# Kernel optimization log

Measured on AMD Instinct MI355X. Metric: run time of the kernel, lower is better.

Reference implementation:

```python
import jax, jax.numpy as jnp
import numpy as np

# Channel schedule of FPSRefineNet(num_structure_points=64, in_channel=640, out=False):
# 640->512 (ReLU), 512->256 (ReLU), 256->128 (ReLU), 128->64 (ReLU since out=False)
CH = [640, 512, 256, 128, 64]
BN_EPS = 1e-5


def _conv_bn_relu(x, W, b, g, beta, m, v):
    # 1x1 Conv2d over [B,C,K,S] == channel matmul; BN in eval mode (running stats);
    # dropout is identity in eval.
    x = jnp.einsum('oc,bcks->boks', W, x) + b[None, :, None, None]
    inv = g / jnp.sqrt(v + BN_EPS)
    x = x * inv[None, :, None, None] + (beta - m * inv)[None, :, None, None]
    return jax.nn.relu(x)


def setup_inputs() -> dict:
    key = jax.random.key(0)
    ks = jax.random.split(key, 32)
    d = {}
    d['grouped_xyz'] = jax.random.normal(ks[0], (8, 3, 32, 1024), jnp.float32)
    d['grouped_points'] = jax.random.normal(ks[1], (8, 640, 32, 1024), jnp.float32)
    i = 2
    for li, (cin, cout) in enumerate(zip(CH[:-1], CH[1:])):
        d[f'W{li}'] = jax.random.normal(ks[i], (cout, cin), jnp.float32) / np.sqrt(cin).astype(np.float32); i += 1
        d[f'b{li}'] = jnp.zeros((cout,), jnp.float32)
        d[f'g{li}'] = jnp.ones((cout,), jnp.float32)
        d[f'beta{li}'] = jnp.zeros((cout,), jnp.float32)
        d[f'm{li}'] = 0.1 * jax.random.normal(ks[i], (cout,), jnp.float32); i += 1
        d[f'v{li}'] = 1.0 + 0.1 * jax.random.uniform(ks[i], (cout,), jnp.float32); i += 1
    return d


def reference(grouped_xyz, grouped_points,
              W0, b0, g0, beta0, m0, v0,
              W1, b1, g1, beta1, m1, v1,
              W2, b2, g2, beta2, m2, v2,
              W3, b3, g3, beta3, m3, v3):
    params = [(W0, b0, g0, beta0, m0, v0),
              (W1, b1, g1, beta1, m1, v1),
              (W2, b2, g2, beta2, m2, v2),
              (W3, b3, g3, beta3, m3, v3)]
    x = grouped_points  # [B, 640, K, S]
    for (W, b, g, be, m, v) in params:
        x = _conv_bn_relu(x, W, b, g, be, m, v)
    # softmax over K (dim=2)
    p = jax.nn.softmax(x, axis=2)  # [B, D'=64, K, S]
    # fused weighted sum over K: sum_k p[b,d,k,s]*xyz[b,c,k,s] -> [B, C, D', S]
    offset_xyz = jnp.einsum('bdks,bcks->bcds', p, grouped_xyz)
    return offset_xyz
```

## Files before the change

### kernel.cpp

```cpp
#include <hip/hip_runtime.h>

typedef unsigned short u16;
typedef __attribute__((ext_vector_type(8))) short bf16x8;
typedef __attribute__((ext_vector_type(4))) float f32x4;
typedef __attribute__((ext_vector_type(16))) float f32x16;

__device__ __forceinline__ u16 f2bf(float f) {
  union { float f; unsigned u; } x; x.f = f;
  return (u16)((x.u + 0x7FFFu + ((x.u >> 16) & 1u)) >> 16);
}
__device__ __forceinline__ float bf2f(u16 h) {
  union { unsigned u; float f; } x; x.u = ((unsigned)h) << 16; return x.f;
}
__device__ __forceinline__ unsigned cvtpk(float lo, float hi) {
  unsigned r;
  asm("v_cvt_pk_bf16_f32 %0, %1, %2" : "=v"(r) : "v"(lo), "v"(hi));
  return r;
}


__global__ __launch_bounds__(256) void prep_kernel(
    const float* __restrict__ W0, const float* __restrict__ W1,
    const float* __restrict__ W2, const float* __restrict__ W3,
    const float* __restrict__ b0, const float* __restrict__ g0, const float* __restrict__ be0, const float* __restrict__ m0, const float* __restrict__ v0,
    const float* __restrict__ b1, const float* __restrict__ g1, const float* __restrict__ be1, const float* __restrict__ m1, const float* __restrict__ v1,
    const float* __restrict__ b2, const float* __restrict__ g2, const float* __restrict__ be2, const float* __restrict__ m2, const float* __restrict__ v2,
    const float* __restrict__ b3, const float* __restrict__ g3, const float* __restrict__ be3, const float* __restrict__ m3, const float* __restrict__ v3,
    u16* __restrict__ Wb, float* __restrict__ sc, float* __restrict__ sh)
{
  int i = blockIdx.x * 256 + threadIdx.x;
  if (i < 62464) {
    const float* Ws; int CIN, KS, local, dstb; bool f16 = false;
    if (i < 40960)      { local = i;         Ws = W0; CIN = 640; KS = 40; dstb = 0; }
    else if (i < 57344) { local = i - 40960; Ws = W1; CIN = 512; KS = 32; dstb = 327680; }
    else if (i < 61440) { local = i - 57344; Ws = W2; CIN = 256; KS = 16; dstb = 458752; }
    else                { local = i - 61440; Ws = W3; CIN = 128; KS = 4;  dstb = 491520; f16 = true; }
    int lane = local & 63, fi = local >> 6;
    int ks = fi % KS, mt = fi / KS;
    int row, k;
    if (!f16) { row = mt * 32 + (lane & 31); k = ks * 16 + (lane >> 5) * 8; }
    else      { row = mt * 16 + (lane & 15); k = ks * 32 + (lane >> 4) * 8; }
    const float* s = Ws + (size_t)row * CIN + k;
    bf16x8 pk;
    #pragma unroll
    for (int j = 0; j < 8; ++j) pk[j] = (short)f2bf(s[j]);
    *reinterpret_cast<bf16x8*>(Wb + dstb + (size_t)local * 8) = pk;
  }
  if (i < 960) {
    const float *B, *G, *BE, *M, *V; int c;
    if (i < 512)      { c = i;       B = b0; G = g0; BE = be0; M = m0; V = v0; }
    else if (i < 768) { c = i - 512; B = b1; G = g1; BE = be1; M = m1; V = v1; }
    else if (i < 896) { c = i - 768; B = b2; G = g2; BE = be2; M = m2; V = v2; }
    else              { c = i - 896; B = b3; G = g3; BE = be3; M = m3; V = v3; }
    float inv = G[c] / sqrtf(V[c] + 1e-5f);
    sc[i] = inv;
    sh[i] = (B[c] - M[c]) * inv + BE[c];
  }
}

template<int MT, int NT>
__device__ __forceinline__ void store_act32(f32x16 (&acc)[MT][NT],
    const float* __restrict__ sc, const float* __restrict__ sh,
    int mrow0, int ntb, int lane, u16* __restrict__ dst, int rowB)
{
  const int l31 = lane & 31, khalf = lane >> 5;
  #pragma unroll
  for (int mi = 0; mi < MT; ++mi) {
    #pragma unroll
    for (int rq = 0; rq < 4; ++rq) {
      const int ch0 = mrow0 + mi * 32 + rq * 8 + khalf * 4;
      const f32x4 s4 = *reinterpret_cast<const f32x4*>(sc + ch0);
      const f32x4 h4 = *reinterpret_cast<const f32x4*>(sh + ch0);
      #pragma unroll
      for (int nt = 0; nt < NT; ++nt) {
        const int px = (ntb + nt) * 32 + l31;
        float r0 = fmaxf(acc[mi][nt][rq * 4 + 0] * s4[0] + h4[0], 0.f);
        float r1 = fmaxf(acc[mi][nt][rq * 4 + 1] * s4[1] + h4[1], 0.f);
        float r2 = fmaxf(acc[mi][nt][rq * 4 + 2] * s4[2] + h4[2], 0.f);
        float r3 = fmaxf(acc[mi][nt][rq * 4 + 3] * s4[3] + h4[3], 0.f);
        uint2 pk;
        pk.x = cvtpk(r0, r1);
        pk.y = cvtpk(r2, r3);
        const unsigned byte = ((unsigned)(px * rowB + ch0 * 2)) ^ ((unsigned)((px & 7) << 4));
        *reinterpret_cast<uint2*>(reinterpret_cast<char*>(dst) + byte) = pk;
      }
    }
  }
}

__device__ __forceinline__ void load8(const float* __restrict__ gbase, int choff, float (&v)[8]) {
  const float* s = gbase + (size_t)choff * 32768u;
  #pragma unroll
  for (int kk = 0; kk < 8; ++kk) v[kk] = s[(size_t)kk * 32768u];
}
__device__ __forceinline__ void write8(float (&v)[8], char* __restrict__ buf, unsigned wb) {
  uint4 pk;
  pk.x = cvtpk(v[0], v[1]);
  pk.y = cvtpk(v[2], v[3]);
  pk.z = cvtpk(v[4], v[5]);
  pk.w = cvtpk(v[6], v[7]);
  *reinterpret_cast<uint4*>(buf + wb) = pk;
}

#define P0_HALF(XB, c, ks0) { \
  __builtin_amdgcn_s_setprio(1); \
  _Pragma("unroll") \
  for (int ksl = 0; ksl < 4; ++ksl) { \
    const int ks = (ks0) + ksl; \
    const unsigned base = ((unsigned)(l31 * 256 + ks * 32 + khalf * 16)) ^ sw; \
    bf16x8 bb0 = *reinterpret_cast<const bf16x8*>((XB) + base); \
    bf16x8 bb1 = *reinterpret_cast<const bf16x8*>((XB) + base + 8192); \
    const int slot = ks & 1; \
    acc0[0][0] = __builtin_amdgcn_mfma_f32_32x32x16_bf16(ar0[slot], bb0, acc0[0][0], 0, 0, 0); \
    acc0[0][1] = __builtin_amdgcn_mfma_f32_32x32x16_bf16(ar0[slot], bb1, acc0[0][1], 0, 0, 0); \
    acc0[1][0] = __builtin_amdgcn_mfma_f32_32x32x16_bf16(ar1[slot], bb0, acc0[1][0], 0, 0, 0); \
    acc0[1][1] = __builtin_amdgcn_mfma_f32_32x32x16_bf16(ar1[slot], bb1, acc0[1][1], 0, 0, 0); \
    const int g_ = (c) * 8 + ks + 2; \
    if (g_ < 40) { \
      ar0[slot] = *reinterpret_cast<const bf16x8*>(A0 + g_ * 512); \
      ar1[slot] = *reinterpret_cast<const bf16x8*>(A1 + g_ * 512); \
    } \
  } \
  __builtin_amdgcn_s_setprio(0); \
}

__global__ __launch_bounds__(512, 4) void fused4_kernel(
    const float* __restrict__ gp, const u16* __restrict__ Wb,
    const float* __restrict__ sc, const float* __restrict__ sh,
    u16* __restrict__ x3)
{
  __shared__ u16 smem[32768];
  char* XsA = reinterpret_cast<char*>(smem);
  char* XsB = XsA + 16384;
  u16*  Y0s = smem;

  const int tid  = threadIdx.x;
  const int lane = tid & 63;
  const int w    = tid >> 6;
  const int l31  = lane & 31, khalf = lane >> 5;
  const unsigned sw = (unsigned)((l31 & 7) << 4);

  const int b  = blockIdx.x >> 9;
  const int jt = blockIdx.x & 511;
  const int j0 = jt << 6;

  const float* gbase = gp + (size_t)b * (640u * 32768u) + (unsigned)(j0 + lane);
  const unsigned wbH0 = ((unsigned)(lane * 256 + w * 16)) ^ ((unsigned)((lane & 7) << 4));
  const unsigned wbH1 = wbH0 + 128;

  const u16* A0 = Wb + (size_t)(2 * w) * (40 * 512) + lane * 8;
  const u16* A1 = A0 + (size_t)(40 * 512);

  float vA[8], vB[8];
  bf16x8 ar0[2], ar1[2];
  f32x16 acc0[2][2] = {};

  load8(gbase, 0 * 128 + 0 * 64 + w * 8, vA);
  load8(gbase, 0 * 128 + 1 * 64 + w * 8, vB);
  ar0[0] = *reinterpret_cast<const bf16x8*>(A0 + 0 * 512);
  ar1[0] = *reinterpret_cast<const bf16x8*>(A1 + 0 * 512);
  ar0[1] = *reinterpret_cast<const bf16x8*>(A0 + 1 * 512);
  ar1[1] = *reinterpret_cast<const bf16x8*>(A1 + 1 * 512);
  write8(vA, XsA, wbH0);
  write8(vB, XsA, wbH1);
  __syncthreads();

  #pragma unroll 1
  for (int c = 0; c < 5; ++c) {
    char* bufc = (c & 1) ? XsB : XsA;
    char* bufn = (c & 1) ? XsA : XsB;
    if (c < 4) {
      load8(gbase, (c + 1) * 128 + 0 * 64 + w * 8, vA);
      load8(gbase, (c + 1) * 128 + 1 * 64 + w * 8, vB);
    }
    P0_HALF(bufc, c, 0);
    if (c < 4) write8(vA, bufn, wbH0);
    P0_HALF(bufc, c, 4);
    if (c < 4) write8(vB, bufn, wbH1);
    __syncthreads();
  }

  store_act32<2, 2>(acc0, sc, sh, w * 64, 0, lane, Y0s, 1024);
  __syncthreads();

  {
    f32x16 acc1[1][2] = {};
    const u16* A = Wb + 327680 + (size_t)w * (32 * 512) + lane * 8;
    bf16x8 ar8[8];
    #pragma unroll
    for (int q = 0; q < 8; ++q) ar8[q] = *reinterpret_cast<const bf16x8*>(A + q * 512);
    __builtin_amdgcn_s_setprio(1);
    #pragma unroll
    for (int ks = 0; ks < 32; ++ks) {
      const unsigned kb = (unsigned)(ks * 32 + khalf * 16);
      bf16x8 bb0 = *reinterpret_cast<const bf16x8*>(reinterpret_cast<const char*>(Y0s) + (((unsigned)(l31 * 1024) + kb) ^ sw));
      bf16x8 bb1 = *reinterpret_cast<const bf16x8*>(reinterpret_cast<const char*>(Y0s) + (((unsigned)((l31 + 32) * 1024) + kb) ^ sw));
      acc1[0][0] = __builtin_amdgcn_mfma_f32_32x32x16_bf16(ar8[ks & 7], bb0, acc1[0][0], 0, 0, 0);
      acc1[0][1] = __builtin_amdgcn_mfma_f32_32x32x16_bf16(ar8[ks & 7], bb1, acc1[0][1], 0, 0, 0);
      if (ks < 24) ar8[ks & 7] = *reinterpret_cast<const bf16x8*>(A + (ks + 8) * 512);
    }
    __builtin_amdgcn_s_setprio(0);
    __syncthreads();
    store_act32<1, 2>(acc1, sc + 512, sh + 512, w * 32, 0, lane, Y0s, 512);
    __syncthreads();
  }

  {
    f32x16 acc2[1][1] = {};
    const u16* A = Wb + 458752 + (size_t)(w & 3) * (16 * 512) + lane * 8;
    const int pxb = (w >> 2) * 32;
    bf16x8 ar8[8];
    #pragma unroll
    for (int q = 0; q < 8; ++q) ar8[q] = *reinterpret_cast<const bf16x8*>(A + q * 512);
    __builtin_amdgcn_s_setprio(1);
    #pragma unroll
    for (int ks = 0; ks < 16; ++ks) {
      const unsigned kb = (unsigned)(ks * 32 + khalf * 16);
      bf16x8 bb0 = *reinterpret_cast<const bf16x8*>(reinterpret_cast<const char*>(Y0s) + (((unsigned)((pxb + l31) * 512) + kb) ^ sw));
      acc2[0][0] = __builtin_amdgcn_mfma_f32_32x32x16_bf16(ar8[ks & 7], bb0, acc2[0][0], 0, 0, 0);
      if (ks < 8) ar8[ks & 7] = *reinterpret_cast<const bf16x8*>(A + (ks + 8) * 512);
    }
    __builtin_amdgcn_s_setprio(0);
    store_act32<1, 1>(acc2, sc + 768, sh + 768, (w & 3) * 32, w >> 2, lane, smem + 16384, 256);
    __syncthreads();
  }

  {
    const int r16 = lane & 15, g = lane >> 4;
    f32x4 acc3[2] = {};
    const u16* A = Wb + 491520 + (size_t)(w & 3) * (4 * 512) + lane * 8;
    bf16x8 a4[4];
    #pragma unroll
    for (int q = 0; q < 4; ++q) a4[q] = *reinterpret_cast<const bf16x8*>(A + q * 512);
    const int ntb = (w >> 2) * 2;
    __builtin_amdgcn_s_setprio(1);
    #pragma unroll
    for (int ks = 0; ks < 4; ++ks) {
      #pragma unroll
      for (int nt = 0; nt < 2; ++nt) {
        const int px = (ntb + nt) * 16 + r16;
        const unsigned byte = ((unsigned)(px * 256 + ks * 64 + g * 16)) ^ ((unsigned)((px & 7) << 4));
        bf16x8 bb = *reinterpret_cast<const bf16x8*>(reinterpret_cast<const char*>(smem) + 32768 + byte);
        acc3[nt] = __builtin_amdgcn_mfma_f32_16x16x32_bf16(a4[ks], bb, acc3[nt], 0, 0, 0);
      }
    }
    __builtin_amdgcn_s_setprio(0);
    const int c0 = (w & 3) * 16 + g * 4;
    const f32x4 s4 = *reinterpret_cast<const f32x4*>(sc + 896 + c0);
    const f32x4 h4 = *reinterpret_cast<const f32x4*>(sh + 896 + c0);
    u16* x3b = x3 + ((size_t)b << 21) + j0;
    #pragma unroll
    for (int nt = 0; nt < 2; ++nt) {
      const int n = (ntb + nt) * 16 + r16;
      #pragma unroll
      for (int r = 0; r < 4; ++r) {
        float vv = fmaxf(acc3[nt][r] * s4[r] + h4[r], 0.f);
        x3b[(size_t)(c0 + r) * 32768 + n] = f2bf(vv);
      }
    }
  }
}

__global__ __launch_bounds__(256) void softmax_ws_kernel(
    const u16* __restrict__ x3, const float* __restrict__ xyz,
    float* __restrict__ out)
{
  const int tid = blockIdx.x * 256 + threadIdx.x;
  const int b = tid >> 15;
  const int rem = tid & 32767;
  const int d = rem >> 9;
  const int s0 = (rem & 511) * 2;

  const u16* xp = x3 + ((size_t)(b * 64 + d) << 15) + s0;
  float pa[32], pb[32];
  float mxa = -1e30f, mxb = -1e30f;
  #pragma unroll
  for (int k = 0; k < 32; ++k) {
    const unsigned u = *reinterpret_cast<const unsigned*>(xp + ((size_t)k << 10));
    const float va = bf2f((u16)(u & 0xFFFFu));
    const float vb = bf2f((u16)(u >> 16));
    pa[k] = va; pb[k] = vb;
    mxa = fmaxf(mxa, va); mxb = fmaxf(mxb, vb);
  }
  float sa = 0.f, sb = 0.f;
  #pragma unroll
  for (int k = 0; k < 32; ++k) {
    pa[k] = __expf(pa[k] - mxa); sa += pa[k];
    pb[k] = __expf(pb[k] - mxb); sb += pb[k];
  }
  const float inva = 1.0f / sa, invb = 1.0f / sb;

  const float* zp = xyz + (size_t)b * (3 * 32768) + s0;
  #pragma unroll
  for (int c = 0; c < 3; ++c) {
    float ax = 0.f, ay = 0.f;
    #pragma unroll
    for (int k = 0; k < 32; ++k) {
      const float2 z = *reinterpret_cast<const float2*>(zp + c * 32768 + (k << 10));
      ax += pa[k] * z.x; ay += pb[k] * z.y;
    }
    float2 o; o.x = ax * inva; o.y = ay * invb;
    *reinterpret_cast<float2*>(out + ((size_t)((b * 3 + c) * 64 + d) << 10) + s0) = o;
  }
}

extern "C" void kernel_launch(void* const* d_in, const int* in_sizes, int n_in,
                              void* d_out, int out_size, void* d_ws, size_t ws_size,
                              hipStream_t stream) {
  const float* xyz = (const float*)d_in[0];
  const float* gp  = (const float*)d_in[1];
  const float* W0 = (const float*)d_in[2];
  const float* W1 = (const float*)d_in[8];
  const float* W2 = (const float*)d_in[14];
  const float* W3 = (const float*)d_in[20];

  char* ws = (char*)d_ws;
  u16*   Wb = (u16*)ws;
  float* sc = (float*)(ws + 999424);
  float* sh = (float*)(ws + 1003264);
  u16*   x3 = (u16*)(ws + 1007104);

  prep_kernel<<<245, 256, 0, stream>>>(
      W0, W1, W2, W3,
      (const float*)d_in[3],  (const float*)d_in[4],  (const float*)d_in[5],  (const float*)d_in[6],  (const float*)d_in[7],
      (const float*)d_in[9],  (const float*)d_in[10], (const float*)d_in[11], (const float*)d_in[12], (const float*)d_in[13],
      (const float*)d_in[15], (const float*)d_in[16], (const float*)d_in[17], (const float*)d_in[18], (const float*)d_in[19],
      (const float*)d_in[21], (const float*)d_in[22], (const float*)d_in[23], (const float*)d_in[24], (const float*)d_in[25],
      Wb, sc, sh);

  fused4_kernel<<<4096, 512, 0, stream>>>(gp, Wb, sc, sh, x3);

  softmax_ws_kernel<<<1024, 256, 0, stream>>>(x3, xyz, (float*)d_out);
}
```

Baseline: 362.8 us.

## Retile layer-1 GEMM across waves and use LDS-only barriers

Layer 1 of the fused MLP is now split so each wave owns two 32-row output tiles over one 32-pixel half, rather than one output tile over all 64 pixels. Each B fragment read from LDS now feeds two MFMAs, and the weight fragments are prefetched through a two-deep register ring instead of eight slots, which halves LDS reads and lowers register pressure. Several __syncthreads calls are replaced with a barrier that waits only on LDS counters (lgkmcnt), so outstanding global loads can stay in flight across it. The risk is that global weight loads are now issued just two steps ahead, which may expose their latency.

```diff
diff --git a/kernel.cpp b/kernel.cpp
--- a/kernel.cpp
+++ b/kernel.cpp
@@ -16,6 +16,12 @@
   unsigned r;
   asm("v_cvt_pk_bf16_f32 %0, %1, %2" : "=v"(r) : "v"(lo), "v"(hi));
   return r;
+}
+__device__ __forceinline__ void bar_ds() {
+  asm volatile("s_waitcnt lgkmcnt(0)" ::: "memory");
+  __builtin_amdgcn_sched_barrier(0);
+  __builtin_amdgcn_s_barrier();
+  __builtin_amdgcn_sched_barrier(0);
 }
 
 
@@ -163,7 +169,7 @@
   ar1[1] = *reinterpret_cast<const bf16x8*>(A1 + 1 * 512);
   write8(vA, XsA, wbH0);
   write8(vB, XsA, wbH1);
-  __syncthreads();
+  bar_ds();
 
   #pragma unroll 1
   for (int c = 0; c < 5; ++c) {
@@ -177,32 +183,39 @@
     if (c < 4) write8(vA, bufn, wbH0);
     P0_HALF(bufc, c, 4);
     if (c < 4) write8(vB, bufn, wbH1);
-    __syncthreads();
+    bar_ds();
   }
 
   store_act32<2, 2>(acc0, sc, sh, w * 64, 0, lane, Y0s, 1024);
-  __syncthreads();
+  bar_ds();
 
   {
-    f32x16 acc1[1][2] = {};
-    const u16* A = Wb + 327680 + (size_t)w * (32 * 512) + lane * 8;
-    bf16x8 ar8[8];
-    #pragma unroll
-    for (int q = 0; q < 8; ++q) ar8[q] = *reinterpret_cast<const bf16x8*>(A + q * 512);
+    f32x16 acc1[2][1] = {};
+    const u16* B0 = Wb + 327680 + (size_t)((w & 3) * 2) * (32 * 512) + lane * 8;
+    const u16* B1 = B0 + 32 * 512;
+    const int pxb = (w >> 2) * 32;
+    bf16x8 br0[2], br1[2];
+    br0[0] = *reinterpret_cast<const bf16x8*>(B0 + 0 * 512);
+    br1[0] = *reinterpret_cast<const bf16x8*>(B1 + 0 * 512);
+    br0[1] = *reinterpret_cast<const bf16x8*>(B0 + 1 * 512);
+    br1[1] = *reinterpret_cast<const bf16x8*>(B1 + 1 * 512);
     __builtin_amdgcn_s_setprio(1);
     #pragma unroll
     for (int ks = 0; ks < 32; ++ks) {
       const unsigned kb = (unsigned)(ks * 32 + khalf * 16);
-      bf16x8 bb0 = *reinterpret_cast<const bf16x8*>(reinterpret_cast<const char*>(Y0s) + (((unsigned)(l31 * 1024) + kb) ^ sw));
-      bf16x8 bb1 = *reinterpret_cast<const bf16x8*>(reinterpret_cast<const char*>(Y0s) + (((unsigned)((l31 + 32) * 1024) + kb) ^ sw));
-      acc1[0][0] = __builtin_amdgcn_mfma_f32_32x32x16_bf16(ar8[ks & 7], bb0, acc1[0][0], 0, 0, 0);
-      acc1[0][1] = __builtin_amdgcn_mfma_f32_32x32x16_bf16(ar8[ks & 7], bb1, acc1[0][1], 0, 0, 0);
-      if (ks < 24) ar8[ks & 7] = *reinterpret_cast<const bf16x8*>(A + (ks + 8) * 512);
+      bf16x8 bb = *reinterpret_cast<const bf16x8*>(reinterpret_cast<const char*>(Y0s) + (((unsigned)((pxb + l31) * 1024) + kb) ^ sw));
+      const int slot = ks & 1;
+      acc1[0][0] = __builtin_amdgcn_mfma_f32_32x32x16_bf16(br0[slot], bb, acc1[0][0], 0, 0, 0);
+      acc1[1][0] = __builtin_amdgcn_mfma_f32_32x32x16_bf16(br1[slot], bb, acc1[1][0], 0, 0, 0);
+      if (ks < 30) {
+        br0[slot] = *reinterpret_cast<const bf16x8*>(B0 + (ks + 2) * 512);
+        br1[slot] = *reinterpret_cast<const bf16x8*>(B1 + (ks + 2) * 512);
+      }
     }
     __builtin_amdgcn_s_setprio(0);
-    __syncthreads();
-    store_act32<1, 2>(acc1, sc + 512, sh + 512, w * 32, 0, lane, Y0s, 512);
-    __syncthreads();
+    bar_ds();
+    store_act32<2, 1>(acc1, sc + 512, sh + 512, (w & 3) * 64, w >> 2, lane, Y0s, 512);
+    bar_ds();
   }
 
   {
@@ -222,7 +235,7 @@
     }
     __builtin_amdgcn_s_setprio(0);
     store_act32<1, 1>(acc2, sc + 768, sh + 768, (w & 3) * 32, w >> 2, lane, smem + 16384, 256);
-    __syncthreads();
+    bar_ds();
   }
 
   {
```

New measurement: 381.4 us. +5.1%, slower.
